# Performance work log

Measured on AMD Instinct MI355X. Metric: run time of the kernel, lower is better.

Reference implementation:

```python
import jax, jax.numpy as jnp
import numpy as np
import math

N, T, D, H = 64, 128, 512, 1024

def setup_inputs() -> dict:
    key = jax.random.key(0)
    ks = jax.random.split(key, 5)
    x = jax.random.normal(ks[0], (N, T, D), dtype=jnp.float32)
    A = jax.random.normal(ks[1], (N, H, 4, 4), dtype=jnp.float32)
    Wx = jax.random.normal(ks[2], (D, 4 * H), dtype=jnp.float32) / math.sqrt(D)
    Wh = jax.random.normal(ks[3], (H, 4 * H), dtype=jnp.float32) / math.sqrt(H)
    Wattn = jax.random.normal(ks[4], (H, 4 * H), dtype=jnp.float32) / math.sqrt(H)
    b = jnp.zeros((4 * H,), dtype=jnp.float32)
    return {"x": x, "A": A, "Wx": Wx, "Wh": Wh, "Wattn": Wattn, "b": b}

def reference(x, A, Wx, Wh, Wattn, b):
    n, t, d = x.shape
    h_dim = A.shape[1]
    L = A.shape[2] * A.shape[3]  # 16 spatial locations
    Af = A.reshape(n, h_dim, L)                      # (N, H, 16)
    h0 = jnp.mean(Af, axis=-1)                       # mean over 4x4 -> (N, H)
    c0 = h0
    inv_sqrt_h = 1.0 / math.sqrt(h_dim)

    def step(carry, xt):
        prev_h, prev_c = carry
        # scaled dot-product attention over 16 locations
        scores = jnp.einsum('nh,nhl->nl', prev_h, Af) * inv_sqrt_h  # (N, 16)
        w = jax.nn.softmax(scores, axis=1)
        attn = jnp.einsum('nhl,nl->nh', Af, w)                      # (N, H)
        # LSTM gates
        a = xt @ Wx + prev_h @ Wh + attn @ Wattn + b                # (N, 4H)
        i, f, o, g = jnp.split(a, 4, axis=1)
        i, f, o = jax.nn.sigmoid(i), jax.nn.sigmoid(f), jax.nn.sigmoid(o)
        g = jnp.tanh(g)
        next_c = f * prev_c + i * g
        next_h = o * jnp.tanh(next_c)
        return (next_h, next_c), next_h

    xs = jnp.swapaxes(x, 0, 1)                       # (T, N, D)
    _, hs = jax.lax.scan(step, (h0, c0), xs)         # hs: (T, N, H)
    return jnp.swapaxes(hs, 0, 1)                    # (N, T, H)
```

## Files before the change

### kernel.cpp

```cpp
#include <hip/hip_runtime.h>
#include <stdint.h>


#define Tt 128
#define FH 4096
#define RING_D 32

typedef __bf16 bf8 __attribute__((ext_vector_type(8)));
typedef float f4 __attribute__((ext_vector_type(4)));
typedef short s8v __attribute__((ext_vector_type(8)));
typedef unsigned long long ull;

__device__ __forceinline__ float bf2f(unsigned short u) {
    union { unsigned u32; float f; } x; x.u32 = ((unsigned)u) << 16; return x.f;
}
__device__ __forceinline__ unsigned short f2bf(float f) {
    union { float f32; unsigned u; } x; x.f32 = f;
    unsigned r = x.u + 0x7fffu + ((x.u >> 16) & 1u);
    return (unsigned short)(r >> 16);
}
__device__ __forceinline__ ull ald(const ull* p) {
    return __hip_atomic_load((ull*)p, __ATOMIC_RELAXED, __HIP_MEMORY_SCOPE_AGENT);
}
__device__ __forceinline__ void ast(ull* p, ull v) {
    __hip_atomic_store(p, v, __ATOMIC_RELAXED, __HIP_MEMORY_SCOPE_AGENT);
}
__device__ __forceinline__ int aldi(const int* p) {
    return __hip_atomic_load((int*)p, __ATOMIC_RELAXED, __HIP_MEMORY_SCOPE_AGENT);
}
__device__ __forceinline__ void asti(int* p, int v) {
    __hip_atomic_store(p, v, __ATOMIC_RELAXED, __HIP_MEMORY_SCOPE_AGENT);
}
__device__ __forceinline__ void astf(float* p, float v) {
    __hip_atomic_store(p, v, __ATOMIC_RELAXED, __HIP_MEMORY_SCOPE_AGENT);
}


__global__ __launch_bounds__(256) void k_cast_bf16(const float* __restrict__ in,
                                                   unsigned short* __restrict__ out, int n) {
    int i = blockIdx.x * 256 + threadIdx.x;
    if (i < n) out[i] = f2bf(in[i]);
}

__global__ __launch_bounds__(256) void k_transpose_bf16(const float* __restrict__ W,
                                                        unsigned short* __restrict__ WT, int K) {
    __shared__ float tl[32][33];
    int c0 = blockIdx.x * 32, k0 = blockIdx.y * 32;
    int tx = threadIdx.x & 31, ty = threadIdx.x >> 5;
    #pragma unroll
    for (int i = 0; i < 32; i += 8) tl[ty + i][tx] = W[(size_t)(k0 + ty + i) * 4096 + c0 + tx];
    __syncthreads();
    #pragma unroll
    for (int i = 0; i < 32; i += 8) WT[(size_t)(c0 + ty + i) * K + k0 + tx] = f2bf(tl[tx][ty + i]);
}

__global__ __launch_bounds__(256) void k_afl(const float* __restrict__ A,
                                             unsigned short* __restrict__ Afl) {
    int idx = blockIdx.x * 256 + threadIdx.x;
    int k = idx & 1023, l = (idx >> 10) & 15, n = idx >> 14;
    Afl[idx] = f2bf(A[((size_t)n * 1024 + k) * 16 + l]);
}

__global__ __launch_bounds__(256) void k_init(const float* __restrict__ A,
                                              float* __restrict__ cstate,
                                              unsigned short* __restrict__ ring0) {
    int idx = blockIdx.x * 256 + threadIdx.x;
    const float* ap = A + (size_t)idx * 16;
    float s = 0.f;
    #pragma unroll
    for (int l = 0; l < 16; l++) s += ap[l];
    float h = s * (1.0f / 16.0f);
    cstate[idx] = h;
    ring0[idx] = f2bf(h);
}

__global__ __launch_bounds__(256) void k_gemm(const unsigned short* __restrict__ A,
                                              const unsigned short* __restrict__ BT,
                                              const float* __restrict__ bias,
                                              unsigned short* __restrict__ out,
                                              int M, int Nn, int K, int mode) {
    __shared__ unsigned short As[128][40];
    __shared__ unsigned short Bs[128][40];
    int m0 = blockIdx.y * 128, n0 = blockIdx.x * 128;
    int tid = threadIdx.x, lane = tid & 63, wave = tid >> 6;
    int wr = wave >> 1, wc = wave & 1, quad = lane >> 4, l16 = lane & 15;
    f4 acc[4][4];
    #pragma unroll
    for (int i = 0; i < 4; i++)
        #pragma unroll
        for (int j = 0; j < 4; j++) acc[i][j] = f4{0.f, 0.f, 0.f, 0.f};

    for (int k0 = 0; k0 < K; k0 += 32) {
        __syncthreads();
        #pragma unroll
        for (int i = 0; i < 2; i++) {
            int idx = i * 256 + tid, r = idx >> 2, c = idx & 3;
            *(s8v*)&As[r][c * 8] = *(const s8v*)&A[(size_t)(m0 + r) * K + k0 + c * 8];
            *(s8v*)&Bs[r][c * 8] = *(const s8v*)&BT[(size_t)(n0 + r) * K + k0 + c * 8];
        }
        __syncthreads();
        bf8 af[4], bfr[4];
        #pragma unroll
        for (int i = 0; i < 4; i++) af[i] = *(const bf8*)&As[wr * 64 + i * 16 + l16][quad * 8];
        #pragma unroll
        for (int j = 0; j < 4; j++) bfr[j] = *(const bf8*)&Bs[wc * 64 + j * 16 + l16][quad * 8];
        #pragma unroll
        for (int i = 0; i < 4; i++)
            #pragma unroll
            for (int j = 0; j < 4; j++)
                acc[i][j] = __builtin_amdgcn_mfma_f32_16x16x32_bf16(af[i], bfr[j], acc[i][j], 0, 0, 0);
    }

    #pragma unroll
    for (int i = 0; i < 4; i++)
        #pragma unroll
        for (int j = 0; j < 4; j++) {
            int row0 = m0 + wr * 64 + i * 16 + quad * 4;
            int col = n0 + wc * 64 + j * 16 + l16;
            float bia = bias ? bias[col] : 0.0f;
            #pragma unroll
            for (int r = 0; r < 4; r++) {
                float v = acc[i][j][r] + bia;
                int rw = row0 + r;
                if (mode == 0) {
                    out[(size_t)rw * Nn + col] = f2bf(v);
                } else if (mode == 1) {
                    int n = rw >> 4, l = rw & 15;
                    out[((size_t)n * Nn + col) * 16 + l] = f2bf(v);
                } else {
                    int n = rw >> 7, t = rw & 127;
                    out[((size_t)t * 64 + n) * Nn + col] = f2bf(v);
                }
            }
        }
}

__global__ __launch_bounds__(512, 2) void k_recur(
    const unsigned short* __restrict__ Afl,
    const unsigned short* __restrict__ WhT, const unsigned short* __restrict__ xwx,
    const unsigned short* __restrict__ P2, const float* __restrict__ cstate,
    unsigned short* __restrict__ ring,
    float* __restrict__ wbuf,
    int* __restrict__ wflag, int* __restrict__ hflag,
    float* __restrict__ out) {
    __shared__ unsigned short WhS[32][1024];
    __shared__ unsigned short hS[32][1024];
    __shared__ float aL[32][36];
    __shared__ float wL[512];
    __shared__ unsigned short hpk[32][8];

    const int wid = blockIdx.x;
    const int R = wid >> 7, C = wid & 127;
    const int tid = threadIdx.x, lane = tid & 63, wave = tid >> 6;
    const int l16 = lane & 15, quad = lane >> 4;
    ull* wbuf_u = (ull*)wbuf;

    const int ntile = wave & 1, ctile = (wave >> 1) & 1;
    const int n_l = tid >> 3, j = tid & 7;
    const int n_glob = R * 32 + n_l;
    const int jcol = C * 8 + j;
    const bool sduty = (C < 8) && (wave >= 4);
    const int srow_l = C * 4 + (wave - 4);
    const int sn = R * 32 + srow_l;

    for (int c = tid; c < 4096; c += 512) {
        int row = c >> 7, pos = c & 127;
        int q = row >> 3, jj = row & 7;
        int acolg = q * 1024 + C * 8 + jj;
        s8v v = *(const s8v*)&WhT[(size_t)acolg * 1024 + pos * 8];
        int e = (pos * 8) ^ ((row & 7) << 3);
        *(s8v*)&WhS[row][e] = v;
    }

    float creg = (tid < 256) ? cstate[(size_t)n_glob * 1024 + jcol] : 0.f;

    __syncthreads();

    for (int t = 0; t < Tt; ++t) {
        const unsigned short* rg = ring + (size_t)(t & (RING_D - 1)) * 65536;
        unsigned short* rw = ring + (size_t)((t + 1) & (RING_D - 1)) * 65536;

        unsigned short xwr[4];
        s8v p2r[4][2];
        if (tid < 256) {
            const unsigned short* xp = xwx + ((size_t)t * 64 + n_glob) * FH;
            #pragma unroll
            for (int q = 0; q < 4; q++) {
                int ac = q * 1024 + jcol;
                xwr[q] = xp[ac];
                const unsigned short* pp = P2 + ((size_t)n_glob * FH + ac) * 16;
                p2r[q][0] = *(const s8v*)pp;
                p2r[q][1] = *(const s8v*)(pp + 8);
            }
        }

        if (t > 0 && tid < 128) {
            while (aldi(&hflag[(R * 128 + tid) * 32]) < t)
                __builtin_amdgcn_s_sleep(2);
        }
        __syncthreads();
        __builtin_amdgcn_fence(__ATOMIC_ACQUIRE, "workgroup");

        #pragma unroll
        for (int it = 0; it < 8; ++it) {
            int c = it * 512 + tid;
            int row = c >> 7, pos = c & 127;
            s8v v = *(const s8v*)&rg[((size_t)(R * 32 + row)) * 1024 + pos * 8];
            int e = (pos * 8) ^ ((row & 7) << 3);
            *(s8v*)&hS[row][e] = v;
        }
        __syncthreads();

        if (wave < 4) {
            const int arow = ntile * 16 + l16;
            const int brow = ctile * 16 + l16;
            const int aswz = (arow & 7) << 3, bswz = (brow & 7) << 3;
            const int kb = quad * 8;
            f4 acc = {0.f, 0.f, 0.f, 0.f};
            #pragma unroll 8
            for (int ks = 0; ks < 32; ++ks) {
                bf8 a = *(const bf8*)&hS[arow][(kb + ks * 32) ^ aswz];
                bf8 b = *(const bf8*)&WhS[brow][(kb + ks * 32) ^ bswz];
                acc = __builtin_amdgcn_mfma_f32_16x16x32_bf16(a, b, acc, 0, 0, 0);
            }
            #pragma unroll
            for (int r = 0; r < 4; r++)
                aL[ntile * 16 + quad * 4 + r][ctile * 16 + l16] = acc[r];
        } else if (sduty) {
            const int sl = lane & 15, kg = lane >> 4;
            const int swz = (srow_l & 7) << 3;
            const unsigned short* ap = Afl + ((size_t)sn * 16 + sl) * 1024 + kg * 256;
            float psum = 0.f;
            #pragma unroll 8
            for (int kc = 0; kc < 32; ++kc) {
                int kbase = kg * 256 + kc * 8;
                s8v hv = *(const s8v*)&hS[srow_l][kbase ^ swz];
                s8v av = *(const s8v*)&ap[kc * 8];
                #pragma unroll
                for (int e2 = 0; e2 < 8; e2++)
                    psum = fmaf(bf2f((unsigned short)hv[e2]),
                                bf2f((unsigned short)av[e2]), psum);
            }
            psum += __shfl_xor(psum, 16, 64);
            psum += __shfl_xor(psum, 32, 64);
            float sc = psum * (1.0f / 32.0f);
            float mx = sc;
            mx = fmaxf(mx, __shfl_xor(mx, 1, 64));
            mx = fmaxf(mx, __shfl_xor(mx, 2, 64));
            mx = fmaxf(mx, __shfl_xor(mx, 4, 64));
            mx = fmaxf(mx, __shfl_xor(mx, 8, 64));
            float ev = __expf(sc - mx);
            float sum = ev;
            sum += __shfl_xor(sum, 1, 64);
            sum += __shfl_xor(sum, 2, 64);
            sum += __shfl_xor(sum, 4, 64);
            sum += __shfl_xor(sum, 8, 64);
            float w = ev / sum;
            if (lane < 16) astf(&wbuf[sn * 16 + sl], w);
        }
        __syncthreads();
        if (C < 8 && tid == 0) asti(&wflag[(R * 8 + C) * 32], t + 1);

        if (tid < 8) {
            while (aldi(&wflag[(R * 8 + tid) * 32]) < t + 1)
                __builtin_amdgcn_s_sleep(2);
        }
        __syncthreads();
        __builtin_amdgcn_fence(__ATOMIC_ACQUIRE, "workgroup");
        if (tid < 256) {
            union { ull u; float f[2]; } cv;
            cv.u = ald(wbuf_u + (size_t)R * 256 + tid);
            wL[tid * 2] = cv.f[0]; wL[tid * 2 + 1] = cv.f[1];
        }
        __syncthreads();

        if (tid < 256) {
            float av4[4];
            #pragma unroll
            for (int q = 0; q < 4; q++) {
                int al = q * 8 + j;
                float v = aL[n_l][al] + bf2f(xwr[q]);
                float sa = 0.f;
                #pragma unroll
                for (int l = 0; l < 8; l++)
                    sa = fmaf(wL[n_l * 16 + l], bf2f((unsigned short)p2r[q][0][l]), sa);
                #pragma unroll
                for (int l = 0; l < 8; l++)
                    sa = fmaf(wL[n_l * 16 + 8 + l], bf2f((unsigned short)p2r[q][1][l]), sa);
                av4[q] = v + sa;
            }
            float ig = 1.f / (1.f + __expf(-av4[0]));
            float fg = 1.f / (1.f + __expf(-av4[1]));
            float og = 1.f / (1.f + __expf(-av4[2]));
            float gg = tanhf(av4[3]);
            creg = fg * creg + ig * gg;
            float hv = og * tanhf(creg);
            out[((size_t)n_glob * Tt + t) * 1024 + jcol] = hv;
            hpk[n_l][j] = f2bf(hv);
        }
        __syncthreads();

        if (t < Tt - 1) {
            if (tid < 64) {
                int row = tid >> 1, half = tid & 1;
                ull v = *(const ull*)&hpk[row][half * 4];
                ast((ull*)rw + ((size_t)(R * 32 + row) << 8) + C * 2 + half, v);
            }
            __syncthreads();
            if (tid == 0) asti(&hflag[wid * 32], t + 1);
        }
    }
}


extern "C" void kernel_launch(void* const* d_in, const int* in_sizes, int n_in,
                              void* d_out, int out_size, void* d_ws, size_t ws_size,
                              hipStream_t stream) {
    const float* x     = (const float*)d_in[0];
    const float* A     = (const float*)d_in[1];
    const float* Wx    = (const float*)d_in[2];
    const float* Wh    = (const float*)d_in[3];
    const float* Wattn = (const float*)d_in[4];
    const float* b     = (const float*)d_in[5];
    float* out = (float*)d_out;
    char* ws = (char*)d_ws;

    unsigned short* xbf    = (unsigned short*)(ws);
    unsigned short* P2     = (unsigned short*)(ws);
    unsigned short* WxT    = (unsigned short*)(ws + 8388608);
    unsigned short* WhT    = (unsigned short*)(ws + 12582912);
    unsigned short* WattnT = (unsigned short*)(ws + 20971520);
    unsigned short* ring   = (unsigned short*)(ws + 20971520);
    unsigned short* Afl    = (unsigned short*)(ws + 29360128);
    unsigned short* xwx    = (unsigned short*)(ws + 31457280);
    float* cstate          = (float*)(ws + 98566144);
    float* wbuf            = (float*)(ws + 99090432);
    int* hflag             = (int*)(ws + 99094528);
    int* wflag             = (int*)(ws + 99127296);

    (void)hipMemsetAsync(ws + 99094528, 0, 36864, stream);

    k_cast_bf16<<<16384, 256, 0, stream>>>(x, xbf, 4194304);
    k_transpose_bf16<<<dim3(128, 16), 256, 0, stream>>>(Wx, WxT, 512);
    k_transpose_bf16<<<dim3(128, 32), 256, 0, stream>>>(Wh, WhT, 1024);
    k_transpose_bf16<<<dim3(128, 32), 256, 0, stream>>>(Wattn, WattnT, 1024);
    k_afl<<<4096, 256, 0, stream>>>(A, Afl);

    k_gemm<<<dim3(32, 64), 256, 0, stream>>>(xbf, WxT, b, xwx, 8192, 4096, 512, 2);
    k_gemm<<<dim3(32, 8), 256, 0, stream>>>(Afl, WattnT, nullptr, P2, 1024, 4096, 1024, 1);

    k_init<<<256, 256, 0, stream>>>(A, cstate, ring);

    k_recur<<<256, 512, 0, stream>>>(Afl, WhT, xwx, P2, cstate, ring, wbuf,
                                     wflag, hflag, out);
}
```

Measured before the change: 1.226 ms.

## Pack attention weights with step tags to replace flag-based cross-block sync

Each softmax weight is now stored as a 64-bit word that also holds the step index. Consumers poll their own two words until the tag matches, which replaces the separate per-group flag write, the flag polling and an extra barrier. The h publish path also drops a block barrier: the storing wave waits on its own vector-memory counter and then raises the flag. This cuts synchronisation latency on the recurrent critical path. The cost is more polling threads and a reliance on relaxed atomics with waitcnt for ordering, which is subtle with respect to memory-model correctness.

```diff
diff --git a/kernel.cpp b/kernel.cpp
--- a/kernel.cpp
+++ b/kernel.cpp
@@ -29,9 +29,6 @@
     return __hip_atomic_load((int*)p, __ATOMIC_RELAXED, __HIP_MEMORY_SCOPE_AGENT);
 }
 __device__ __forceinline__ void asti(int* p, int v) {
-    __hip_atomic_store(p, v, __ATOMIC_RELAXED, __HIP_MEMORY_SCOPE_AGENT);
-}
-__device__ __forceinline__ void astf(float* p, float v) {
     __hip_atomic_store(p, v, __ATOMIC_RELAXED, __HIP_MEMORY_SCOPE_AGENT);
 }
 
@@ -140,8 +137,8 @@
     const unsigned short* __restrict__ WhT, const unsigned short* __restrict__ xwx,
     const unsigned short* __restrict__ P2, const float* __restrict__ cstate,
     unsigned short* __restrict__ ring,
-    float* __restrict__ wbuf,
-    int* __restrict__ wflag, int* __restrict__ hflag,
+    ull* __restrict__ wE,
+    int* __restrict__ hflag,
     float* __restrict__ out) {
     __shared__ unsigned short WhS[32][1024];
     __shared__ unsigned short hS[32][1024];
@@ -153,7 +150,6 @@
     const int R = wid >> 7, C = wid & 127;
     const int tid = threadIdx.x, lane = tid & 63, wave = tid >> 6;
     const int l16 = lane & 15, quad = lane >> 4;
-    ull* wbuf_u = (ull*)wbuf;
 
     const int ntile = wave & 1, ctile = (wave >> 1) & 1;
     const int n_l = tid >> 3, j = tid & 7;
@@ -256,21 +252,32 @@
             sum += __shfl_xor(sum, 4, 64);
             sum += __shfl_xor(sum, 8, 64);
             float w = ev / sum;
-            if (lane < 16) astf(&wbuf[sn * 16 + sl], w);
-        }
-        __syncthreads();
-        if (C < 8 && tid == 0) asti(&wflag[(R * 8 + C) * 32], t + 1);
-
-        if (tid < 8) {
-            while (aldi(&wflag[(R * 8 + tid) * 32]) < t + 1)
+            if (lane < 16) {
+                union { ull u; unsigned v[2]; } pk;
+                union { float f; unsigned b; } wb; wb.f = w;
+                pk.v[0] = wb.b;
+                pk.v[1] = (unsigned)(t + 1);
+                ast(&wE[(size_t)sn * 16 + sl], pk.u);
+            }
+        }
+        __syncthreads();
+
+        if (tid < 256) {
+            const size_t wb = (size_t)n_glob * 16 + j * 2;
+            ull a0, a1;
+            for (;;) {
+                a0 = ald(&wE[wb]);
+                if ((unsigned)(a0 >> 32) >= (unsigned)(t + 1)) break;
                 __builtin_amdgcn_s_sleep(2);
-        }
-        __syncthreads();
-        __builtin_amdgcn_fence(__ATOMIC_ACQUIRE, "workgroup");
-        if (tid < 256) {
-            union { ull u; float f[2]; } cv;
-            cv.u = ald(wbuf_u + (size_t)R * 256 + tid);
-            wL[tid * 2] = cv.f[0]; wL[tid * 2 + 1] = cv.f[1];
+            }
+            for (;;) {
+                a1 = ald(&wE[wb + 1]);
+                if ((unsigned)(a1 >> 32) >= (unsigned)(t + 1)) break;
+                __builtin_amdgcn_s_sleep(2);
+            }
+            union { unsigned b; float f; } w0, w1;
+            w0.b = (unsigned)a0; w1.b = (unsigned)a1;
+            wL[tid * 2] = w0.f; wL[tid * 2 + 1] = w1.f;
         }
         __syncthreads();
 
@@ -305,9 +312,9 @@
                 int row = tid >> 1, half = tid & 1;
                 ull v = *(const ull*)&hpk[row][half * 4];
                 ast((ull*)rw + ((size_t)(R * 32 + row) << 8) + C * 2 + half, v);
-            }
-            __syncthreads();
-            if (tid == 0) asti(&hflag[wid * 32], t + 1);
+                asm volatile("s_waitcnt vmcnt(0)" ::: "memory");
+                if (tid == 0) asti(&hflag[wid * 32], t + 1);
+            }
         }
     }
 }
@@ -334,11 +341,11 @@
     unsigned short* Afl    = (unsigned short*)(ws + 29360128);
     unsigned short* xwx    = (unsigned short*)(ws + 31457280);
     float* cstate          = (float*)(ws + 98566144);
-    float* wbuf            = (float*)(ws + 99090432);
+    ull* wE                = (ull*)(ws + 98828288);
     int* hflag             = (int*)(ws + 99094528);
-    int* wflag             = (int*)(ws + 99127296);
-
-    (void)hipMemsetAsync(ws + 99094528, 0, 36864, stream);
+
+    (void)hipMemsetAsync(ws + 98828288, 0, 8192, stream);
+    (void)hipMemsetAsync(ws + 99094528, 0, 32768, stream);
 
     k_cast_bf16<<<16384, 256, 0, stream>>>(x, xbf, 4194304);
     k_transpose_bf16<<<dim3(128, 16), 256, 0, stream>>>(Wx, WxT, 512);
@@ -351,6 +358,6 @@
 
     k_init<<<256, 256, 0, stream>>>(A, cstate, ring);
 
-    k_recur<<<256, 512, 0, stream>>>(Afl, WhT, xwx, P2, cstate, ring, wbuf,
-                                     wflag, hflag, out);
-}
+    k_recur<<<256, 512, 0, stream>>>(Afl, WhT, xwx, P2, cstate, ring, wE,
+                                     hflag, out);
+}
```

Measured after the change: 1.276 ms. +4.1%, slower.
